# Optimization experiments

Hardware: AMD Instinct MI355X
Metric: run time of the kernel (lower is better)

The kernel has to match this reference:

```python
import jax, jax.numpy as jnp
import numpy as np

# Fixed Sobel kernels, OIHW [1,1,3,3]
_SOBEL_X = jnp.array([[-1.0, 0.0, 1.0], [-2.0, 0.0, 2.0], [-1.0, 0.0, 1.0]], dtype=jnp.float32).reshape(1, 1, 3, 3)
_SOBEL_Y = jnp.array([[1.0, 2.0, 1.0], [0.0, 0.0, 0.0], [-1.0, -2.0, -1.0]], dtype=jnp.float32).reshape(1, 1, 3, 3)


def _conv(x, k):
    # x: [B,1,H,W], k: [1,1,3,3], stride 1, padding 1 (SAME)
    return jax.lax.conv_general_dilated(
        x, k.astype(x.dtype), window_strides=(1, 1), padding=((1, 1), (1, 1)),
        dimension_numbers=('NCHW', 'OIHW', 'NCHW'))


def _gradient(x):
    return jnp.abs(_conv(x, _SOBEL_X)) + jnp.abs(_conv(x, _SOBEL_Y))


def setup_inputs() -> dict:
    key = jax.random.key(0)
    k1, k2, k3 = jax.random.split(key, 3)
    B, H, W = 32, 512, 512
    return {
        'image_vis': jax.random.uniform(k1, (B, 3, H, W), dtype=jnp.float32),
        'image_ir': jax.random.uniform(k2, (B, 1, H, W), dtype=jnp.float32),
        'generate_img': jax.random.uniform(k3, (B, 3, H, W), dtype=jnp.float32),
    }


def reference(image_vis, image_ir, generate_img):
    loss_weight = 1.0
    image_y = image_vis[:, :1, :, :]
    generate_y = generate_img[:, :1, :, :]
    g_gen = _gradient(generate_y)
    g_vis = _gradient(image_y)
    g_ir = _gradient(image_ir)
    target = jnp.maximum(g_vis, g_ir)
    return loss_weight * jnp.mean(jnp.abs(g_gen - target))
```

## Files before the change

kernel.cpp:

```cpp
#include <hip/hip_runtime.h>


#define IMG_H 512
#define IMG_W 512
#define BATCH 32
#define ROWS 8
#define XT (IMG_W / 4)
#define STRIPS (IMG_H / ROWS)
#define THREADS 256
#define TOTAL_THREADS (BATCH * STRIPS * XT)
#define NBLOCKS (TOTAL_THREADS / THREADS)
#define NPIX ((double)BATCH * IMG_H * IMG_W)

struct Row { float l, x, y, z, w, r; };

__device__ __forceinline__ void zero_row(Row& r) {
    r.l = r.x = r.y = r.z = r.w = r.r = 0.0f;
}

__device__ __forceinline__ void load_row(const float* __restrict__ p, int xb,
                                         bool hl, bool hr, Row& r) {
    float4 v = *reinterpret_cast<const float4*>(p + xb);
    r.x = v.x; r.y = v.y; r.z = v.z; r.w = v.w;
    r.l = hl ? p[xb - 1] : 0.0f;
    r.r = hr ? p[xb + 4] : 0.0f;
}

__device__ __forceinline__ float gete(const Row& r, int j) {
    switch (j) {
        case -1: return r.l;
        case 0:  return r.x;
        case 1:  return r.y;
        case 2:  return r.z;
        case 3:  return r.w;
        default: return r.r;
    }
}

__device__ __forceinline__ float sobel_grad(const Row& t, const Row& m, const Row& b, int j) {
    float a  = gete(t, j - 1), bb = gete(t, j), c  = gete(t, j + 1);
    float d  = gete(m, j - 1),                  f  = gete(m, j + 1);
    float g  = gete(b, j - 1), hh = gete(b, j), i2 = gete(b, j + 1);
    float gx = (c - a) + 2.0f * (f - d) + (i2 - g);
    float gy = (a + 2.0f * bb + c) - (g + 2.0f * hh + i2);
    return fabsf(gx) + fabsf(gy);
}

__global__ __launch_bounds__(THREADS)
void grad_loss_kernel(const float* __restrict__ vis, const float* __restrict__ ir,
                      const float* __restrict__ gen, float* __restrict__ partial) {
    int t    = blockIdx.x * THREADS + threadIdx.x;
    int xt   = t & (XT - 1);
    int rest = t >> 7;
    int ys   = rest & (STRIPS - 1);
    int b    = rest >> 6;

    const float* pv = vis + (size_t)b * 3 * IMG_H * IMG_W;
    const float* pi = ir  + (size_t)b * IMG_H * IMG_W;
    const float* pg = gen + (size_t)b * 3 * IMG_H * IMG_W;

    int  xb = xt * 4;
    bool hl = (xt != 0), hr = (xt != XT - 1);
    int  y0 = ys * ROWS;

    Row v0, v1, v2, i0, i1, i2r, g0, g1, g2;
    if (y0 == 0) {
        zero_row(v0); zero_row(i0); zero_row(g0);
    } else {
        load_row(pv + (size_t)(y0 - 1) * IMG_W, xb, hl, hr, v0);
        load_row(pi + (size_t)(y0 - 1) * IMG_W, xb, hl, hr, i0);
        load_row(pg + (size_t)(y0 - 1) * IMG_W, xb, hl, hr, g0);
    }
    load_row(pv + (size_t)y0 * IMG_W, xb, hl, hr, v1);
    load_row(pi + (size_t)y0 * IMG_W, xb, hl, hr, i1);
    load_row(pg + (size_t)y0 * IMG_W, xb, hl, hr, g1);

    float acc = 0.0f;
    #pragma unroll
    for (int r = 0; r < ROWS; ++r) {
        int y = y0 + r;
        if (y == IMG_H - 1) {
            zero_row(v2); zero_row(i2r); zero_row(g2);
        } else {
            load_row(pv + (size_t)(y + 1) * IMG_W, xb, hl, hr, v2);
            load_row(pi + (size_t)(y + 1) * IMG_W, xb, hl, hr, i2r);
            load_row(pg + (size_t)(y + 1) * IMG_W, xb, hl, hr, g2);
        }
        #pragma unroll
        for (int j = 0; j < 4; ++j) {
            float ggen = sobel_grad(g0, g1, g2, j);
            float gvis = sobel_grad(v0, v1, v2, j);
            float gir  = sobel_grad(i0, i1, i2r, j);
            acc += fabsf(ggen - fmaxf(gvis, gir));
        }
        v0 = v1; v1 = v2;
        i0 = i1; i1 = i2r;
        g0 = g1; g1 = g2;
    }

    #pragma unroll
    for (int off = 32; off > 0; off >>= 1)
        acc += __shfl_down(acc, off, 64);
    __shared__ float s[THREADS / 64];
    int lane = threadIdx.x & 63, wid = threadIdx.x >> 6;
    if (lane == 0) s[wid] = acc;
    __syncthreads();
    if (threadIdx.x == 0)
        partial[blockIdx.x] = s[0] + s[1] + s[2] + s[3];
}

__global__ __launch_bounds__(THREADS)
void reduce_kernel(const float* __restrict__ partial, float* __restrict__ out) {
    float acc = 0.0f;
    for (int i = threadIdx.x; i < NBLOCKS; i += THREADS)
        acc += partial[i];
    #pragma unroll
    for (int off = 32; off > 0; off >>= 1)
        acc += __shfl_down(acc, off, 64);
    __shared__ float s[THREADS / 64];
    int lane = threadIdx.x & 63, wid = threadIdx.x >> 6;
    if (lane == 0) s[wid] = acc;
    __syncthreads();
    if (threadIdx.x == 0)
        out[0] = (float)((s[0] + s[1] + s[2] + s[3]) * (1.0 / NPIX));
}

extern "C" void kernel_launch(void* const* d_in, const int* in_sizes, int n_in,
                              void* d_out, int out_size, void* d_ws, size_t ws_size,
                              hipStream_t stream) {
    const float* vis = (const float*)d_in[0];
    const float* ir  = (const float*)d_in[1];
    const float* gen = (const float*)d_in[2];
    float* out       = (float*)d_out;
    float* partial   = (float*)d_ws;

    grad_loss_kernel<<<NBLOCKS, THREADS, 0, stream>>>(vis, ir, gen, partial);
    reduce_kernel<<<1, THREADS, 0, stream>>>(partial, out);
}
```

Before: 26.40 us.

## Fuse final reduction via last-block atomic counter and double rows per thread

Replaces the separate reduce kernel with a last-block-done pattern: each block publishes its partial with release semantics, increments a global counter, and the final block sums all partials and writes the mean. Each thread now also processes 16 rows instead of 8, which halves the block count and cuts the redundant halo row loads. The second kernel launch is dropped, but a memset launch is added to reset the counter. Fewer threads in flight may reduce the latency hiding available for the loads.

Measured after the change: 45.00 us. 70.5% more time.

```diff
diff --git a/kernel.cpp b/kernel.cpp
--- a/kernel.cpp
+++ b/kernel.cpp
@@ -4,7 +4,7 @@
 #define IMG_H 512
 #define IMG_W 512
 #define BATCH 32
-#define ROWS 8
+#define ROWS 16
 #define XT (IMG_W / 4)
 #define STRIPS (IMG_H / ROWS)
 #define THREADS 256
@@ -48,12 +48,13 @@
 
 __global__ __launch_bounds__(THREADS)
 void grad_loss_kernel(const float* __restrict__ vis, const float* __restrict__ ir,
-                      const float* __restrict__ gen, float* __restrict__ partial) {
+                      const float* __restrict__ gen, float* __restrict__ partial,
+                      unsigned* __restrict__ counter, float* __restrict__ out) {
     int t    = blockIdx.x * THREADS + threadIdx.x;
     int xt   = t & (XT - 1);
     int rest = t >> 7;
     int ys   = rest & (STRIPS - 1);
-    int b    = rest >> 6;
+    int b    = rest >> 5;
 
     const float* pv = vis + (size_t)b * 3 * IMG_H * IMG_W;
     const float* pi = ir  + (size_t)b * IMG_H * IMG_W;
@@ -102,27 +103,36 @@
     for (int off = 32; off > 0; off >>= 1)
         acc += __shfl_down(acc, off, 64);
     __shared__ float s[THREADS / 64];
+    __shared__ bool is_last;
     int lane = threadIdx.x & 63, wid = threadIdx.x >> 6;
     if (lane == 0) s[wid] = acc;
     __syncthreads();
-    if (threadIdx.x == 0)
-        partial[blockIdx.x] = s[0] + s[1] + s[2] + s[3];
-}
 
-__global__ __launch_bounds__(THREADS)
-void reduce_kernel(const float* __restrict__ partial, float* __restrict__ out) {
-    float acc = 0.0f;
-    for (int i = threadIdx.x; i < NBLOCKS; i += THREADS)
-        acc += partial[i];
-    #pragma unroll
-    for (int off = 32; off > 0; off >>= 1)
-        acc += __shfl_down(acc, off, 64);
-    __shared__ float s[THREADS / 64];
-    int lane = threadIdx.x & 63, wid = threadIdx.x >> 6;
-    if (lane == 0) s[wid] = acc;
+    if (threadIdx.x == 0) {
+        float blocksum = s[0] + s[1] + s[2] + s[3];
+        __hip_atomic_store(&partial[blockIdx.x], blocksum,
+                           __ATOMIC_RELEASE, __HIP_MEMORY_SCOPE_AGENT);
+        unsigned old = __hip_atomic_fetch_add(counter, 1u,
+                           __ATOMIC_ACQ_REL, __HIP_MEMORY_SCOPE_AGENT);
+        is_last = (old == NBLOCKS - 1);
+    }
     __syncthreads();
-    if (threadIdx.x == 0)
-        out[0] = (float)((s[0] + s[1] + s[2] + s[3]) * (1.0 / NPIX));
+
+    if (is_last) {
+        float a = 0.0f;
+        #pragma unroll
+        for (int i = 0; i < NBLOCKS / THREADS; ++i)
+            a += __hip_atomic_load(&partial[threadIdx.x + i * THREADS],
+                                   __ATOMIC_RELAXED, __HIP_MEMORY_SCOPE_AGENT);
+        #pragma unroll
+        for (int off = 32; off > 0; off >>= 1)
+            a += __shfl_down(a, off, 64);
+        __shared__ float s2[THREADS / 64];
+        if (lane == 0) s2[wid] = a;
+        __syncthreads();
+        if (threadIdx.x == 0)
+            out[0] = (float)((s2[0] + s2[1] + s2[2] + s2[3]) * (1.0 / NPIX));
+    }
 }
 
 extern "C" void kernel_launch(void* const* d_in, const int* in_sizes, int n_in,
@@ -133,7 +143,8 @@
     const float* gen = (const float*)d_in[2];
     float* out       = (float*)d_out;
     float* partial   = (float*)d_ws;
+    unsigned* counter = (unsigned*)((char*)d_ws + 4096);
 
-    grad_loss_kernel<<<NBLOCKS, THREADS, 0, stream>>>(vis, ir, gen, partial);
-    reduce_kernel<<<1, THREADS, 0, stream>>>(partial, out);
+    hipMemsetAsync(counter, 0, sizeof(unsigned), stream);
+    grad_loss_kernel<<<NBLOCKS, THREADS, 0, stream>>>(vis, ir, gen, partial, counter, out);
 }
```
